# Kernel tuning notes

Hardware: AMD Instinct MI355X
Metric: run time of the kernel (lower is better)

Reference implementation:

```python
import jax, jax.numpy as jnp
import numpy as np

T, B, IN, H = 512, 64, 1024, 1024

def setup_inputs() -> dict:
    key = jax.random.key(0)
    ks = jax.random.split(key, 7)
    X = jax.random.normal(ks[0], (T, B, IN), dtype=jnp.float32)
    h0 = jax.random.normal(ks[1], (B, H), dtype=jnp.float32)
    c0 = jax.random.normal(ks[2], (B, H), dtype=jnp.float32)
    mask = jax.random.randint(ks[3], (T, B), 0, 2, dtype=jnp.int32)
    # orthogonal-ish init approximated with scaled normal (math is identical at runtime)
    W_x_ifoc = jax.random.normal(ks[4], (4 * H, IN), dtype=jnp.float32) / np.sqrt(IN)
    W_h_ifoc = jax.random.normal(ks[5], (4 * H, H), dtype=jnp.float32) / np.sqrt(H)
    b_ifoc = jnp.zeros((4 * H,), dtype=jnp.float32)
    return {"X": X, "h0": h0, "c0": c0, "mask": mask,
            "W_x_ifoc": W_x_ifoc, "W_h_ifoc": W_h_ifoc, "b_ifoc": b_ifoc}

def reference(X, h0, c0, mask, W_x_ifoc, W_h_ifoc, b_ifoc):
    Hd = h0.shape[-1]
    # precompute input projection for all timesteps: [T, B, 4H]
    X4 = jnp.einsum('tbi,gi->tbg', X, W_x_ifoc) + b_ifoc
    m_f = mask.astype(X.dtype)[..., None]  # [T, B, 1]

    def step(carry, inp):
        pre_h, pre_c = carry
        x4, m = inp
        # NOTE: recurrent matmul is applied to the CELL state (non-standard)
        pre = x4 + pre_c @ W_h_ifoc.T  # [B, 4H]
        i, f, o, g = jnp.split(pre, 4, axis=-1)
        i = jax.nn.sigmoid(i)
        f = jax.nn.sigmoid(f)
        o = jax.nn.sigmoid(o)
        c = f * pre_c + i * jnp.tanh(g)
        h = o * jnp.tanh(c)
        h = h * m + pre_h * (1 - m)
        c = c * m + pre_c * (1 - m)
        return (h, c), h

    (h_last, c_last), hiddens = jax.lax.scan(step, (h0, c0), (X4, m_f))
    return hiddens, h_last, c_last
```

## Files before the change

### kernel.cpp

```cpp
#include <hip/hip_runtime.h>
#include <cstdint>
#include <cstddef>

#define T_STEPS 512
#define BATCH   64
#define HD      1024
#define BH      (BATCH * HD)
#define NBLK    256
#define NSG     4
#define BSG     16
#define JBLK    16

using half8   = __attribute__((ext_vector_type(8))) _Float16;
using half4   = __attribute__((ext_vector_type(4))) _Float16;
using floatx4 = __attribute__((ext_vector_type(4))) float;
using float4v = __attribute__((ext_vector_type(4))) float;
using u64     = unsigned long long;

__device__ __forceinline__ float sigmoidf_(float x) { return 1.0f / (1.0f + __expf(-x)); }

__device__ __forceinline__ half8 cvt_h8(float4v a, float4v b) {
    half8 r;
    r[0] = (_Float16)a[0]; r[1] = (_Float16)a[1];
    r[2] = (_Float16)a[2]; r[3] = (_Float16)a[3];
    r[4] = (_Float16)b[0]; r[5] = (_Float16)b[1];
    r[6] = (_Float16)b[2]; r[7] = (_Float16)b[3];
    return r;
}

__device__ __forceinline__ void st_sc1_b64(_Float16* p, u64 v) {
    asm volatile("global_store_dwordx2 %0, %1, off sc0 sc1"
                 :: "v"(p), "v"(v) : "memory");
}

__device__ __forceinline__ u64 pack_lo16(unsigned a, unsigned b, unsigned c, unsigned d) {
    return (u64)(a & 0xffffu) | ((u64)(b & 0xffffu) << 16)
         | ((u64)(c & 0xffffu) << 32) | ((u64)(d & 0xffffu) << 48);
}
__device__ __forceinline__ u64 pack_hi16(unsigned a, unsigned b, unsigned c, unsigned d) {
    return (u64)(a >> 16) | ((u64)(b >> 16) << 16)
         | ((u64)(c >> 16) << 32) | ((u64)(d >> 16) << 48);
}

static const size_t BAR_GRP_OFF  = 0;
static const size_t BAR_ROOT_OFF = 20480;
static const size_t CH_OFF  = 24576;
static const size_t CL_OFF  = CH_OFF + (size_t)2 * BH * 2;
static const size_t WX_OFF  = 1u << 20;
static const size_t WHH_OFF = WX_OFF  + (size_t)8 * 1024 * 1024;
static const size_t WHL_OFF = WHH_OFF + (size_t)8 * 1024 * 1024;
static const size_t XH_OFF  = WHL_OFF + (size_t)8 * 1024 * 1024;
static const size_t X4_OFF  = XH_OFF;
static const size_t TIER_A2_WS = X4_OFF + (size_t)32768 * 4096 * 2;
static const size_t TIER_A_WS  = XH_OFF + (size_t)T_STEPS * BH * 2;
static const size_t TIER_B_WS  = XH_OFF;

__global__ void prep_zero(int* bar) {
    int i = blockIdx.x * 256 + threadIdx.x;
    if (i < 6144) bar[i] = 0;
}

__global__ void prep_w(const float* __restrict__ Wx, const float* __restrict__ Wh,
                       _Float16* __restrict__ wx16,
                       _Float16* __restrict__ whh, _Float16* __restrict__ whl) {
    int i = blockIdx.x * 256 + threadIdx.x;
    if (i < 4 * HD * HD) {
        wx16[i] = (_Float16)Wx[i];
        float w = Wh[i];
        _Float16 h = (_Float16)w;
        whh[i] = h;
        whl[i] = (_Float16)(w - (float)h);
    }
}

__global__ void prep_x(const float* __restrict__ X, _Float16* __restrict__ xh) {
    size_t i = (size_t)blockIdx.x * 256 + threadIdx.x;
    if (i < (size_t)T_STEPS * BH) xh[i] = (_Float16)X[i];
}

__global__ __launch_bounds__(256) void x4_gemm(
    const float* __restrict__ X,
    const _Float16* __restrict__ wx16,
    _Float16* __restrict__ x4)
{
    __shared__ _Float16 sA[128][40];
    __shared__ _Float16 sB[128][40];

    const int tid  = threadIdx.x;
    const int wave = tid >> 6;
    const int lane = tid & 63;
    const int m0 = blockIdx.x * 128, n0 = blockIdx.y * 128;
    const int wm = (wave & 1) * 64,  wn = (wave >> 1) * 64;
    const int fm = lane & 15, q = lane >> 4;

    floatx4 acc[4][4];
    #pragma unroll
    for (int i = 0; i < 4; i++)
        #pragma unroll
        for (int j = 0; j < 4; j++)
            acc[i][j] = (floatx4){0.f, 0.f, 0.f, 0.f};

    for (int k0 = 0; k0 < 1024; k0 += 32) {
        {
            const int kq = (tid & 7) * 4;
            const int rb = tid >> 3;
            #pragma unroll
            for (int it = 0; it < 4; it++) {
                int row = rb + it * 32;
                float4v v = *(const float4v*)(X + (size_t)(m0 + row) * 1024 + k0 + kq);
                half4 h; h[0] = (_Float16)v[0]; h[1] = (_Float16)v[1];
                h[2] = (_Float16)v[2]; h[3] = (_Float16)v[3];
                *(half4*)&sA[row][kq] = h;
            }
        }
        {
            const int half = tid & 1;
            const int row  = tid >> 1;
            const _Float16* src = wx16 + (size_t)(n0 + row) * 1024 + k0 + half * 16;
            *(half8*)&sB[row][half * 16]     = *(const half8*)(src);
            *(half8*)&sB[row][half * 16 + 8] = *(const half8*)(src + 8);
        }
        __syncthreads();

        half8 af[4], bf[4];
        #pragma unroll
        for (int i = 0; i < 4; i++) af[i] = *(const half8*)&sA[wm + 16 * i + fm][q * 8];
        #pragma unroll
        for (int j = 0; j < 4; j++) bf[j] = *(const half8*)&sB[wn + 16 * j + fm][q * 8];
        #pragma unroll
        for (int i = 0; i < 4; i++)
            #pragma unroll
            for (int j = 0; j < 4; j++)
                acc[i][j] = __builtin_amdgcn_mfma_f32_16x16x32_f16(af[i], bf[j], acc[i][j], 0, 0, 0);
        __syncthreads();
    }

    #pragma unroll
    for (int i = 0; i < 4; i++)
        #pragma unroll
        for (int j = 0; j < 4; j++)
            #pragma unroll
            for (int r = 0; r < 4; r++) {
                int row = m0 + wm + 16 * i + q * 4 + r;
                int col = n0 + wn + 16 * j + fm;
                x4[(size_t)row * 4096 + col] = (_Float16)acc[i][j][r];
            }
}

__device__ __forceinline__ void grid_bar(int* grp, int* root, int slot) {
    __syncthreads();
    if (threadIdx.x == 0) {
        int g = blockIdx.x >> 5;
        int v = __hip_atomic_fetch_add(&grp[slot * 8 + g], 1,
                                       __ATOMIC_ACQ_REL, __HIP_MEMORY_SCOPE_AGENT);
        if (v == 31)
            __hip_atomic_fetch_add(&root[slot], 1,
                                   __ATOMIC_ACQ_REL, __HIP_MEMORY_SCOPE_AGENT);
        while (__hip_atomic_load(&root[slot], __ATOMIC_RELAXED,
                                 __HIP_MEMORY_SCOPE_AGENT) < 8)
            __builtin_amdgcn_s_sleep(2);
        (void)__hip_atomic_load(&root[slot], __ATOMIC_ACQUIRE,
                                __HIP_MEMORY_SCOPE_AGENT);
    }
    __syncthreads();
}

__global__ __launch_bounds__(512, 1) void lstm_persist4(
    const _Float16* __restrict__ x4,
    const float* __restrict__ h0, const float* __restrict__ c0,
    const float* __restrict__ bias, const int* __restrict__ mask,
    const _Float16* __restrict__ whh, const _Float16* __restrict__ whl,
    _Float16* __restrict__ chg, _Float16* __restrict__ clg,
    int* __restrict__ bar,
    float* __restrict__ out)
{
    __shared__ float s_pre[8][4][16][18];
    __shared__ float s_h[256], s_c[256];

    const int tid  = threadIdx.x;
    const int wave = tid >> 6;
    const int lane = tid & 63;
    const int sg   = blockIdx.x >> 6;
    const int lb   = blockIdx.x & 63;
    const int b0   = sg * BSG;
    const int j0   = lb * JBLK;

    int*       myflag = bar + (((sg << 6) | lb) << 4);
    const int* pflag  = bar + (((sg << 6) | (wave << 3) | (lane & 7)) << 4);

    const int nn    = lane & 15;
    const int q     = lane >> 4;
    const int kbase = wave * 128 + q * 8;
    const int arow  = lane & 15;

    half8 wh_[4][4], wl_[4][4];
    #pragma unroll
    for (int g = 0; g < 4; g++) {
        const size_t wr = (size_t)(g * HD + j0 + nn) * HD + kbase;
        #pragma unroll
        for (int k = 0; k < 4; k++) {
            wh_[g][k] = *(const half8*)(whh + wr + k * 32);
            wl_[g][k] = *(const half8*)(whl + wr + k * 32);
        }
    }

    float biasr[4] = {0.f, 0.f, 0.f, 0.f};
    float xg[4]    = {0.f, 0.f, 0.f, 0.f};
    int   mv       = 0;
    if (tid < 256) {
        int bl = tid >> 4, n = tid & 15;
        int b = b0 + bl, j = j0 + n;
        float cv = c0[b * HD + j];
        s_c[tid] = cv;
        s_h[tid] = h0[b * HD + j];
        #pragma unroll
        for (int g = 0; g < 4; g++) biasr[g] = bias[g * HD + j];

        _Float16 chi = (_Float16)cv;
        _Float16 clo = (_Float16)(cv - (float)chi);
        unsigned pk = (unsigned)__builtin_bit_cast(unsigned short, chi)
                    | ((unsigned)__builtin_bit_cast(unsigned short, clo) << 16);
        unsigned p1 = __shfl_down(pk, 1);
        unsigned p2 = __shfl_down(pk, 2);
        unsigned p3 = __shfl_down(pk, 3);
        if ((n & 3) == 0) {
            st_sc1_b64(chg + b * HD + j0 + (n & ~3), pack_lo16(pk, p1, p2, p3));
            st_sc1_b64(clg + b * HD + j0 + (n & ~3), pack_hi16(pk, p1, p2, p3));
        }
        #pragma unroll
        for (int g = 0; g < 4; g++)
            xg[g] = (float)x4[(size_t)b * 4096 + g * HD + j];
        mv = mask[b];
        asm volatile("s_waitcnt vmcnt(0)" ::: "memory");
    }
    __syncthreads();
    if (tid == 0)
        __hip_atomic_store(myflag, 1, __ATOMIC_RELAXED, __HIP_MEMORY_SCOPE_AGENT);

    for (int t = 0; t < T_STEPS; t++) {
        const int cur = t & 1;

        const int need = t + 1;
        int fv = __hip_atomic_load(pflag, __ATOMIC_RELAXED, __HIP_MEMORY_SCOPE_AGENT);
        while (!__all(fv >= need)) {
            __builtin_amdgcn_s_sleep(1);
            fv = __hip_atomic_load(pflag, __ATOMIC_RELAXED, __HIP_MEMORY_SCOPE_AGENT);
        }

        const _Float16* chp = chg + (size_t)cur * BH + (size_t)(b0 + arow) * HD + kbase;
        const _Float16* clp = clg + (size_t)cur * BH + (size_t)(b0 + arow) * HD + kbase;

        half8 a0, a1, a2, a3, l0, l1, l2, l3;
        asm volatile(
            "global_load_dwordx4 %0, %8, off sc0 sc1\n\t"
            "global_load_dwordx4 %1, %8, off offset:64 sc0 sc1\n\t"
            "global_load_dwordx4 %2, %8, off offset:128 sc0 sc1\n\t"
            "global_load_dwordx4 %3, %8, off offset:192 sc0 sc1\n\t"
            "global_load_dwordx4 %4, %9, off sc0 sc1\n\t"
            "global_load_dwordx4 %5, %9, off offset:64 sc0 sc1\n\t"
            "global_load_dwordx4 %6, %9, off offset:128 sc0 sc1\n\t"
            "global_load_dwordx4 %7, %9, off offset:192 sc0 sc1\n\t"
            "s_waitcnt vmcnt(0)"
            : "=&v"(a0), "=&v"(a1), "=&v"(a2), "=&v"(a3),
              "=&v"(l0), "=&v"(l1), "=&v"(l2), "=&v"(l3)
            : "v"(chp), "v"(clp)
            : "memory");

        floatx4 acc[4];
        #pragma unroll
        for (int g = 0; g < 4; g++) acc[g] = (floatx4){0.f, 0.f, 0.f, 0.f};
        #pragma unroll
        for (int g = 0; g < 4; g++) {
            floatx4 t0 = acc[g];
            t0 = __builtin_amdgcn_mfma_f32_16x16x32_f16(a0, wh_[g][0], t0, 0, 0, 0);
            t0 = __builtin_amdgcn_mfma_f32_16x16x32_f16(l0, wh_[g][0], t0, 0, 0, 0);
            t0 = __builtin_amdgcn_mfma_f32_16x16x32_f16(a0, wl_[g][0], t0, 0, 0, 0);
            t0 = __builtin_amdgcn_mfma_f32_16x16x32_f16(a1, wh_[g][1], t0, 0, 0, 0);
            t0 = __builtin_amdgcn_mfma_f32_16x16x32_f16(l1, wh_[g][1], t0, 0, 0, 0);
            t0 = __builtin_amdgcn_mfma_f32_16x16x32_f16(a1, wl_[g][1], t0, 0, 0, 0);
            t0 = __builtin_amdgcn_mfma_f32_16x16x32_f16(a2, wh_[g][2], t0, 0, 0, 0);
            t0 = __builtin_amdgcn_mfma_f32_16x16x32_f16(l2, wh_[g][2], t0, 0, 0, 0);
            t0 = __builtin_amdgcn_mfma_f32_16x16x32_f16(a2, wl_[g][2], t0, 0, 0, 0);
            t0 = __builtin_amdgcn_mfma_f32_16x16x32_f16(a3, wh_[g][3], t0, 0, 0, 0);
            t0 = __builtin_amdgcn_mfma_f32_16x16x32_f16(l3, wh_[g][3], t0, 0, 0, 0);
            t0 = __builtin_amdgcn_mfma_f32_16x16x32_f16(a3, wl_[g][3], t0, 0, 0, 0);
            acc[g] = t0;
        }

        #pragma unroll
        for (int g = 0; g < 4; g++) {
            s_pre[wave][g][q * 4 + 0][nn] = acc[g][0];
            s_pre[wave][g][q * 4 + 1][nn] = acc[g][1];
            s_pre[wave][g][q * 4 + 2][nn] = acc[g][2];
            s_pre[wave][g][q * 4 + 3][nn] = acc[g][3];
        }
        __syncthreads();

        float h_out = 0.f, c_out = 0.f;
        if (tid < 256) {
            int bl = tid >> 4, n = tid & 15;
            int b = b0 + bl, j = j0 + n;

            float pg[4];
            #pragma unroll
            for (int g = 0; g < 4; g++) {
                float s = xg[g] + biasr[g];
                #pragma unroll
                for (int kh = 0; kh < 8; kh++)
                    s += s_pre[kh][g][bl][n];
                pg[g] = s;
            }

            float c_old = s_c[tid];
            float i_g = sigmoidf_(pg[0]);
            float f_g = sigmoidf_(pg[1]);
            float o_g = sigmoidf_(pg[2]);
            float g_g = tanhf(pg[3]);
            float c_new = f_g * c_old + i_g * g_g;
            float h_new = o_g * tanhf(c_new);

            h_out = mv ? h_new : s_h[tid];
            c_out = mv ? c_new : c_old;
            s_h[tid] = h_out;
            s_c[tid] = c_out;

            _Float16 chi = (_Float16)c_out;
            _Float16 clo = (_Float16)(c_out - (float)chi);
            unsigned pk = (unsigned)__builtin_bit_cast(unsigned short, chi)
                        | ((unsigned)__builtin_bit_cast(unsigned short, clo) << 16);
            unsigned p1 = __shfl_down(pk, 1);
            unsigned p2 = __shfl_down(pk, 2);
            unsigned p3 = __shfl_down(pk, 3);
            if ((n & 3) == 0) {
                int nxt = cur ^ 1;
                st_sc1_b64(chg + (size_t)nxt * BH + (size_t)b * HD + j0 + (n & ~3),
                           pack_lo16(pk, p1, p2, p3));
                st_sc1_b64(clg + (size_t)nxt * BH + (size_t)b * HD + j0 + (n & ~3),
                           pack_hi16(pk, p1, p2, p3));
            }
            asm volatile("s_waitcnt vmcnt(0)" ::: "memory");
        }
        __syncthreads();
        if (tid == 0)
            __hip_atomic_store(myflag, t + 2, __ATOMIC_RELAXED, __HIP_MEMORY_SCOPE_AGENT);

        if (tid < 256) {
            int bl = tid >> 4, n = tid & 15;
            int b = b0 + bl, j = j0 + n;
            out[(size_t)t * BH + (size_t)b * HD + j] = h_out;
            if (t == T_STEPS - 1) {
                size_t tail = (size_t)T_STEPS * BH;
                out[tail + (size_t)b * HD + j]      = h_out;
                out[tail + BH + (size_t)b * HD + j] = c_out;
            }
            int tn = (t + 1 < T_STEPS) ? t + 1 : t;
            #pragma unroll
            for (int g = 0; g < 4; g++)
                xg[g] = (float)x4[((size_t)tn * BATCH + b) * 4096 + g * HD + j];
            mv = mask[tn * BATCH + b];
        }
    }
}

template<bool XF16>
__global__ __launch_bounds__(1024, 4) void lstm_persist(
    const float* __restrict__ X, const _Float16* __restrict__ xh,
    const float* __restrict__ h0, const float* __restrict__ c0,
    const float* __restrict__ bias, const int* __restrict__ mask,
    const _Float16* __restrict__ wx16, const _Float16* __restrict__ whh,
    const _Float16* __restrict__ whl,
    _Float16* __restrict__ chg, _Float16* __restrict__ clg,
    int* __restrict__ barg, int* __restrict__ barr,
    float* __restrict__ out)
{
    __shared__ _Float16 s_wh[16 * 1032];
    __shared__ float    s_pre[16][16][17];
    __shared__ float    s_h[256], s_c[256];

    const int tid  = threadIdx.x;
    const int wave = tid >> 6;
    const int lane = tid & 63;
    const int j0   = blockIdx.x * 4;

    for (int idx = tid; idx < 2048; idx += 1024) {
        int n  = idx >> 7;
        int kk = (idx & 127) << 3;
        int r  = (n >> 2) * HD + j0 + (n & 3);
        *(half8*)&s_wh[n * 1032 + kk] = *(const half8*)(whh + (size_t)r * HD + kk);
    }

    float biasr[4] = {0.f, 0.f, 0.f, 0.f};
    if (tid < 256) {
        int b = tid >> 2, jj = tid & 3, j = j0 + jj;
        float cv = c0[b * HD + j];
        s_c[tid] = cv;
        s_h[tid] = h0[b * HD + j];
        _Float16 hi = (_Float16)cv;
        chg[b * HD + j] = hi;
        clg[b * HD + j] = (_Float16)(cv - (float)hi);
        #pragma unroll
        for (int g = 0; g < 4; g++) biasr[g] = bias[g * HD + j];
    }
    grid_bar(barg, barr, 0);

    const int mt    = wave & 3;
    const int kh    = wave >> 2;
    const int arow  = mt * 16 + (lane & 15);
    const int nn    = lane & 15;
    const int q     = lane >> 4;
    const int kbase = kh * 256 + q * 8;
    const int wrow  = (nn >> 2) * HD + j0 + (nn & 3);

    const _Float16* wxp = wx16 + (size_t)wrow * HD + kbase;
    const _Float16* wlp = whl  + (size_t)wrow * HD + kbase;
    const _Float16* whp = (const _Float16*)&s_wh[nn * 1032 + kbase];

    for (int t = 0; t < T_STEPS; t++) {
        const int cur = t & 1;
        const _Float16* chp = chg + (size_t)cur * BH + (size_t)arow * HD + kbase;
        const _Float16* clp = clg + (size_t)cur * BH + (size_t)arow * HD + kbase;

        floatx4 acc = {0.f, 0.f, 0.f, 0.f};

        if (XF16) {
            const _Float16* xp = xh + (size_t)t * BH + (size_t)arow * HD + kbase;
            #pragma unroll 4
            for (int k = 0; k < 256; k += 32) {
                half8 av = *(const half8*)(xp + k);
                half8 bv = *(const half8*)(wxp + k);
                acc = __builtin_amdgcn_mfma_f32_16x16x32_f16(av, bv, acc, 0, 0, 0);
            }
        } else {
            const float* xp = X + (size_t)t * BH + (size_t)arow * HD + kbase;
            #pragma unroll 4
            for (int k = 0; k < 256; k += 32) {
                float4v x0 = *(const float4v*)(xp + k);
                float4v x1 = *(const float4v*)(xp + k + 4);
                half8 av = cvt_h8(x0, x1);
                half8 bv = *(const half8*)(wxp + k);
                acc = __builtin_amdgcn_mfma_f32_16x16x32_f16(av, bv, acc, 0, 0, 0);
            }
        }

        #pragma unroll 4
        for (int k = 0; k < 256; k += 32) {
            half8 ah = *(const half8*)(chp + k);
            half8 al = *(const half8*)(clp + k);
            half8 bh = *(const half8*)(whp + k);
            half8 bl = *(const half8*)(wlp + k);
            acc = __builtin_amdgcn_mfma_f32_16x16x32_f16(ah, bh, acc, 0, 0, 0);
            acc = __builtin_amdgcn_mfma_f32_16x16x32_f16(al, bh, acc, 0, 0, 0);
            acc = __builtin_amdgcn_mfma_f32_16x16x32_f16(ah, bl, acc, 0, 0, 0);
        }

        s_pre[wave][q * 4 + 0][nn] = acc[0];
        s_pre[wave][q * 4 + 1][nn] = acc[1];
        s_pre[wave][q * 4 + 2][nn] = acc[2];
        s_pre[wave][q * 4 + 3][nn] = acc[3];
        __syncthreads();

        if (tid < 256) {
            int b = tid >> 2, jj = tid & 3, j = j0 + jj;
            int m = b & 15, mtt = b >> 4;

            float pg[4];
            #pragma unroll
            for (int g = 0; g < 4; g++) {
                float s = 0.f;
                #pragma unroll
                for (int kk = 0; kk < 4; kk++)
                    s += s_pre[kk * 4 + mtt][m][g * 4 + jj];
                pg[g] = s + biasr[g];
            }

            float c_old = s_c[tid];
            float i_g = sigmoidf_(pg[0]);
            float f_g = sigmoidf_(pg[1]);
            float o_g = sigmoidf_(pg[2]);
            float g_g = tanhf(pg[3]);
            float c_new = f_g * c_old + i_g * g_g;
            float h_new = o_g * tanhf(c_new);

            int mv = mask[t * BATCH + b];
            float h_out = mv ? h_new : s_h[tid];
            float c_out = mv ? c_new : c_old;
            s_h[tid] = h_out;
            s_c[tid] = c_out;

            int nxt = cur ^ 1;
            _Float16 hi = (_Float16)c_out;
            chg[(size_t)nxt * BH + b * HD + j] = hi;
            clg[(size_t)nxt * BH + b * HD + j] = (_Float16)(c_out - (float)hi);
            out[(size_t)t * BH + b * HD + j] = h_out;

            if (t == T_STEPS - 1) {
                size_t tail = (size_t)T_STEPS * BH;
                out[tail + b * HD + j]      = h_out;
                out[tail + BH + b * HD + j] = c_out;
            }
        }
        grid_bar(barg, barr, t + 1);
    }
}

__global__ void init_c_fb(const float* __restrict__ c0, float* __restrict__ cf,
                          _Float16* __restrict__ ch, _Float16* __restrict__ cl) {
    int i = blockIdx.x * 256 + threadIdx.x;
    if (i < BH) {
        float v = c0[i];
        cf[i] = v;
        _Float16 h = (_Float16)v;
        ch[i] = h;
        cl[i] = (_Float16)(v - (float)h);
    }
}

__global__ __launch_bounds__(1024) void lstm_step_fb(
    const float* __restrict__ X, const float* __restrict__ h0,
    const float* __restrict__ Wx, const float* __restrict__ Wh,
    const float* __restrict__ bias, const int* __restrict__ mask,
    float* __restrict__ cf, _Float16* __restrict__ chbuf, _Float16* __restrict__ clbuf,
    float* __restrict__ out, int t)
{
    __shared__ float lds_pre[4][64][16];
    const int tid = threadIdx.x, wave = tid >> 6, lane = tid & 63;
    const int g = wave & 3, mt = wave >> 2, j0 = blockIdx.x * 16;
    const int cur = t & 1;
    const float* cf_prev = cf + (size_t)cur * BH;
    const _Float16* ch_prev = chbuf + (size_t)cur * BH;
    const _Float16* cl_prev = clbuf + (size_t)cur * BH;
    float* cf_next = cf + (size_t)(cur ^ 1) * BH;
    _Float16* ch_next = chbuf + (size_t)(cur ^ 1) * BH;
    _Float16* cl_next = clbuf + (size_t)(cur ^ 1) * BH;
    const int arow = mt * 16 + (lane & 15);
    const int brow = g * HD + j0 + (lane & 15);
    const int koff = (lane >> 4) * 8;
    floatx4 acc = {0.f, 0.f, 0.f, 0.f};
    {
        const float* xp = X + (size_t)t * BH + (size_t)arow * HD + koff;
        const float* wp = Wx + (size_t)brow * HD + koff;
        #pragma unroll 4
        for (int k = 0; k < HD; k += 32) {
            float4v x0 = *(const float4v*)(xp + k);
            float4v x1 = *(const float4v*)(xp + k + 4);
            float4v w0 = *(const float4v*)(wp + k);
            float4v w1 = *(const float4v*)(wp + k + 4);
            acc = __builtin_amdgcn_mfma_f32_16x16x32_f16(cvt_h8(x0, x1), cvt_h8(w0, w1), acc, 0, 0, 0);
        }
    }
    {
        const _Float16* chp = ch_prev + (size_t)arow * HD + koff;
        const _Float16* clp = cl_prev + (size_t)arow * HD + koff;
        const float* whp = Wh + (size_t)brow * HD + koff;
        #pragma unroll 4
        for (int k = 0; k < HD; k += 32) {
            half8 ah = *(const half8*)(chp + k);
            half8 al = *(const half8*)(clp + k);
            float4v w0 = *(const float4v*)(whp + k);
            float4v w1 = *(const float4v*)(whp + k + 4);
            half8 bh = cvt_h8(w0, w1);
            float4v r0, r1;
            r0[0] = w0[0] - (float)bh[0]; r0[1] = w0[1] - (float)bh[1];
            r0[2] = w0[2] - (float)bh[2]; r0[3] = w0[3] - (float)bh[3];
            r1[0] = w1[0] - (float)bh[4]; r1[1] = w1[1] - (float)bh[5];
            r1[2] = w1[2] - (float)bh[6]; r1[3] = w1[3] - (float)bh[7];
            half8 bl = cvt_h8(r0, r1);
            acc = __builtin_amdgcn_mfma_f32_16x16x32_f16(ah, bh, acc, 0, 0, 0);
            acc = __builtin_amdgcn_mfma_f32_16x16x32_f16(al, bh, acc, 0, 0, 0);
            acc = __builtin_amdgcn_mfma_f32_16x16x32_f16(ah, bl, acc, 0, 0, 0);
        }
    }
    {
        const int qq = lane >> 4, col = lane & 15;
        lds_pre[g][mt * 16 + qq * 4 + 0][col] = acc[0];
        lds_pre[g][mt * 16 + qq * 4 + 1][col] = acc[1];
        lds_pre[g][mt * 16 + qq * 4 + 2][col] = acc[2];
        lds_pre[g][mt * 16 + qq * 4 + 3][col] = acc[3];
    }
    __syncthreads();
    {
        const int bl2 = tid >> 4, n = tid & 15, j = j0 + n;
        float pg[4];
        #pragma unroll
        for (int gg = 0; gg < 4; gg++) pg[gg] = lds_pre[gg][bl2][n] + bias[gg * HD + j];
        float c_old = cf_prev[bl2 * HD + j];
        float i_g = sigmoidf_(pg[0]), f_g = sigmoidf_(pg[1]);
        float o_g = sigmoidf_(pg[2]), g_g = tanhf(pg[3]);
        float c_new = f_g * c_old + i_g * g_g;
        float h_new = o_g * tanhf(c_new);
        int mv = mask[t * BATCH + bl2];
        float h_prev = (t == 0) ? h0[bl2 * HD + j] : out[(size_t)(t - 1) * BH + bl2 * HD + j];
        float h_out = mv ? h_new : h_prev;
        float c_out = mv ? c_new : c_old;
        cf_next[bl2 * HD + j] = c_out;
        _Float16 hh = (_Float16)c_out;
        ch_next[bl2 * HD + j] = hh;
        cl_next[bl2 * HD + j] = (_Float16)(c_out - (float)hh);
        out[(size_t)t * BH + bl2 * HD + j] = h_out;
        if (t == T_STEPS - 1) {
            size_t tail = (size_t)T_STEPS * BH;
            out[tail + bl2 * HD + j] = h_out;
            out[tail + BH + bl2 * HD + j] = c_out;
        }
    }
}

extern "C" void kernel_launch(void* const* d_in, const int* in_sizes, int n_in,
                              void* d_out, int out_size, void* d_ws, size_t ws_size,
                              hipStream_t stream) {
    const float* X    = (const float*)d_in[0];
    const float* h0   = (const float*)d_in[1];
    const float* c0   = (const float*)d_in[2];
    const int*   mask = (const int*)  d_in[3];
    const float* Wx   = (const float*)d_in[4];
    const float* Wh   = (const float*)d_in[5];
    const float* bias = (const float*)d_in[6];
    float* out = (float*)d_out;
    char* ws = (char*)d_ws;

    if (ws_size >= TIER_B_WS) {
        int*      barg = (int*)(ws + BAR_GRP_OFF);
        int*      barr = (int*)(ws + BAR_ROOT_OFF);
        _Float16* chg  = (_Float16*)(ws + CH_OFF);
        _Float16* clg  = (_Float16*)(ws + CL_OFF);
        _Float16* wx16 = (_Float16*)(ws + WX_OFF);
        _Float16* whh  = (_Float16*)(ws + WHH_OFF);
        _Float16* whl  = (_Float16*)(ws + WHL_OFF);

        prep_zero<<<dim3(24), dim3(256), 0, stream>>>(barg);
        prep_w<<<dim3(16384), dim3(256), 0, stream>>>(Wx, Wh, wx16, whh, whl);

        if (ws_size >= TIER_A2_WS) {
            _Float16* x4 = (_Float16*)(ws + X4_OFF);
            x4_gemm<<<dim3(256, 32), dim3(256), 0, stream>>>(X, wx16, x4);
            void* args[] = {
                (void*)&x4, (void*)&h0, (void*)&c0, (void*)&bias, (void*)&mask,
                (void*)&whh, (void*)&whl, (void*)&chg, (void*)&clg,
                (void*)&barg, (void*)&out
            };
            hipLaunchCooperativeKernel((const void*)&lstm_persist4,
                                       dim3(NBLK), dim3(512), args, 0, stream);
        } else {
            _Float16* xh = (_Float16*)(ws + XH_OFF);
            const bool tierA = ws_size >= TIER_A_WS;
            if (tierA)
                prep_x<<<dim3(131072), dim3(256), 0, stream>>>(X, xh);
            void* args[] = {
                (void*)&X, (void*)&xh, (void*)&h0, (void*)&c0, (void*)&bias,
                (void*)&mask, (void*)&wx16, (void*)&whh, (void*)&whl,
                (void*)&chg, (void*)&clg, (void*)&barg, (void*)&barr, (void*)&out
            };
            if (tierA)
                hipLaunchCooperativeKernel((const void*)&lstm_persist<true>,
                                           dim3(NBLK), dim3(1024), args, 0, stream);
            else
                hipLaunchCooperativeKernel((const void*)&lstm_persist<false>,
                                           dim3(NBLK), dim3(1024), args, 0, stream);
        }
    } else {
        float*    cf = (float*)ws;
        _Float16* ch = (_Float16*)(ws + 524288);
        _Float16* cl = (_Float16*)(ws + 786432);
        init_c_fb<<<dim3((BH + 255) / 256), dim3(256), 0, stream>>>(c0, cf, ch, cl);
        for (int t = 0; t < T_STEPS; t++)
            lstm_step_fb<<<dim3(64), dim3(1024), 0, stream>>>(
                X, h0, Wx, Wh, bias, mask, cf, ch, cl, out, t);
    }
}
```

Before: 3.169 ms.

## Replace per-step flag barrier with parity-tagged cell-state data polling

Removes the per-block flag stores, the flag spin-wait and the trailing __syncthreads/vmcnt wait from each timestep. Instead, the low mantissa bit of each fp16 hi/lo cell value carries the step parity, and consumers poll the data itself until every word shows the expected parity. A triple-buffered interleaved hi/lo state array and double-buffered LDS partials make this safe, and a poison kernel initialises the buffers. The cost is one mantissa bit of precision in each half of the split cell state, plus repeated polling loads of the full operand.

New measurement: 4.087 ms. 1.29x slower.

```diff
diff --git a/kernel.cpp b/kernel.cpp
--- a/kernel.cpp
+++ b/kernel.cpp
@@ -10,11 +10,13 @@
 #define NSG     4
 #define BSG     16
 #define JBLK    16
+#define CBYTES  ((size_t)BH * 4)
 
 using half8   = __attribute__((ext_vector_type(8))) _Float16;
 using half4   = __attribute__((ext_vector_type(4))) _Float16;
 using floatx4 = __attribute__((ext_vector_type(4))) float;
 using float4v = __attribute__((ext_vector_type(4))) float;
+using int4v   = __attribute__((ext_vector_type(4))) int;
 using u64     = unsigned long long;
 
 __device__ __forceinline__ float sigmoidf_(float x) { return 1.0f / (1.0f + __expf(-x)); }
@@ -28,11 +30,6 @@
     return r;
 }
 
-__device__ __forceinline__ void st_sc1_b64(_Float16* p, u64 v) {
-    asm volatile("global_store_dwordx2 %0, %1, off sc0 sc1"
-                 :: "v"(p), "v"(v) : "memory");
-}
-
 __device__ __forceinline__ u64 pack_lo16(unsigned a, unsigned b, unsigned c, unsigned d) {
     return (u64)(a & 0xffffu) | ((u64)(b & 0xffffu) << 16)
          | ((u64)(c & 0xffffu) << 32) | ((u64)(d & 0xffffu) << 48);
@@ -40,6 +37,15 @@
 __device__ __forceinline__ u64 pack_hi16(unsigned a, unsigned b, unsigned c, unsigned d) {
     return (u64)(a >> 16) | ((u64)(b >> 16) << 16)
          | ((u64)(c >> 16) << 32) | ((u64)(d >> 16) << 48);
+}
+
+__device__ __forceinline__ unsigned tag_pack(float c, unsigned p) {
+    unsigned hb = (unsigned)__builtin_bit_cast(unsigned short, (_Float16)c);
+    hb = (hb & 0xFFFEu) | p;
+    _Float16 hf = __builtin_bit_cast(_Float16, (unsigned short)hb);
+    unsigned lb = (unsigned)__builtin_bit_cast(unsigned short, (_Float16)(c - (float)hf));
+    lb = (lb & 0xFFFEu) | p;
+    return hb | (lb << 16);
 }
 
 static const size_t BAR_GRP_OFF  = 0;
@@ -58,6 +64,14 @@
 __global__ void prep_zero(int* bar) {
     int i = blockIdx.x * 256 + threadIdx.x;
     if (i < 6144) bar[i] = 0;
+}
+
+__global__ void prep_poison(unsigned* c3) {
+    int i = blockIdx.x * 256 + threadIdx.x;
+    if (i < 196608) {
+        int buf = i >> 16;
+        c3[i] = (buf == 1) ? 0u : 0x00010001u;
+    }
 }
 
 __global__ void prep_w(const float* __restrict__ Wx, const float* __restrict__ Wh,
@@ -165,16 +179,15 @@
     __syncthreads();
 }
 
-__global__ __launch_bounds__(512, 1) void lstm_persist4(
+__global__ __launch_bounds__(512, 1) void lstm_persist5(
     const _Float16* __restrict__ x4,
     const float* __restrict__ h0, const float* __restrict__ c0,
     const float* __restrict__ bias, const int* __restrict__ mask,
     const _Float16* __restrict__ whh, const _Float16* __restrict__ whl,
-    _Float16* __restrict__ chg, _Float16* __restrict__ clg,
-    int* __restrict__ bar,
+    char* __restrict__ c3,
     float* __restrict__ out)
 {
-    __shared__ float s_pre[8][4][16][18];
+    __shared__ float s_pre[2][8][4][16][18];
     __shared__ float s_h[256], s_c[256];
 
     const int tid  = threadIdx.x;
@@ -184,9 +197,6 @@
     const int lb   = blockIdx.x & 63;
     const int b0   = sg * BSG;
     const int j0   = lb * JBLK;
-
-    int*       myflag = bar + (((sg << 6) | lb) << 4);
-    const int* pflag  = bar + (((sg << 6) | (wave << 3) | (lane & 7)) << 4);
 
     const int nn    = lane & 15;
     const int q     = lane >> 4;
@@ -216,55 +226,71 @@
         #pragma unroll
         for (int g = 0; g < 4; g++) biasr[g] = bias[g * HD + j];
 
-        _Float16 chi = (_Float16)cv;
-        _Float16 clo = (_Float16)(cv - (float)chi);
-        unsigned pk = (unsigned)__builtin_bit_cast(unsigned short, chi)
-                    | ((unsigned)__builtin_bit_cast(unsigned short, clo) << 16);
+        unsigned pk = tag_pack(cv, 0u);
         unsigned p1 = __shfl_down(pk, 1);
         unsigned p2 = __shfl_down(pk, 2);
         unsigned p3 = __shfl_down(pk, 3);
         if ((n & 3) == 0) {
-            st_sc1_b64(chg + b * HD + j0 + (n & ~3), pack_lo16(pk, p1, p2, p3));
-            st_sc1_b64(clg + b * HD + j0 + (n & ~3), pack_hi16(pk, p1, p2, p3));
+            union { u64 qv[2]; int4v v; } sv;
+            sv.qv[0] = pack_lo16(pk, p1, p2, p3);
+            sv.qv[1] = pack_hi16(pk, p1, p2, p3);
+            char* wp = c3 + ((size_t)b * HD + j0 + n) * 4;
+            asm volatile("global_store_dwordx4 %0, %1, off sc0 sc1"
+                         :: "v"(wp), "v"(sv.v) : "memory");
         }
         #pragma unroll
         for (int g = 0; g < 4; g++)
             xg[g] = (float)x4[(size_t)b * 4096 + g * HD + j];
         mv = mask[b];
-        asm volatile("s_waitcnt vmcnt(0)" ::: "memory");
-    }
-    __syncthreads();
-    if (tid == 0)
-        __hip_atomic_store(myflag, 1, __ATOMIC_RELAXED, __HIP_MEMORY_SCOPE_AGENT);
-
+    }
+
+    int bi = 0;
     for (int t = 0; t < T_STEPS; t++) {
-        const int cur = t & 1;
-
-        const int need = t + 1;
-        int fv = __hip_atomic_load(pflag, __ATOMIC_RELAXED, __HIP_MEMORY_SCOPE_AGENT);
-        while (!__all(fv >= need)) {
-            __builtin_amdgcn_s_sleep(1);
-            fv = __hip_atomic_load(pflag, __ATOMIC_RELAXED, __HIP_MEMORY_SCOPE_AGENT);
-        }
-
-        const _Float16* chp = chg + (size_t)cur * BH + (size_t)(b0 + arow) * HD + kbase;
-        const _Float16* clp = clg + (size_t)cur * BH + (size_t)(b0 + arow) * HD + kbase;
-
-        half8 a0, a1, a2, a3, l0, l1, l2, l3;
-        asm volatile(
-            "global_load_dwordx4 %0, %8, off sc0 sc1\n\t"
-            "global_load_dwordx4 %1, %8, off offset:64 sc0 sc1\n\t"
-            "global_load_dwordx4 %2, %8, off offset:128 sc0 sc1\n\t"
-            "global_load_dwordx4 %3, %8, off offset:192 sc0 sc1\n\t"
-            "global_load_dwordx4 %4, %9, off sc0 sc1\n\t"
-            "global_load_dwordx4 %5, %9, off offset:64 sc0 sc1\n\t"
-            "global_load_dwordx4 %6, %9, off offset:128 sc0 sc1\n\t"
-            "global_load_dwordx4 %7, %9, off offset:192 sc0 sc1\n\t"
-            "s_waitcnt vmcnt(0)"
-            : "=&v"(a0), "=&v"(a1), "=&v"(a2), "=&v"(a3),
-              "=&v"(l0), "=&v"(l1), "=&v"(l2), "=&v"(l3)
-            : "v"(chp), "v"(clp)
-            : "memory");
+        const int pp = t & 1;
+        const unsigned pat = pp ? 0x00010001u : 0u;
+
+        int4v u0, u1, u2, u3, u4, u5, u6, u7;
+        const char* cp = c3 + (size_t)bi * CBYTES
+                       + ((size_t)(b0 + arow) * HD + kbase) * 4;
+        for (;;) {
+            asm volatile(
+                "global_load_dwordx4 %0, %8, off sc0 sc1\n\t"
+                "global_load_dwordx4 %1, %8, off offset:16 sc0 sc1\n\t"
+                "global_load_dwordx4 %2, %8, off offset:128 sc0 sc1\n\t"
+                "global_load_dwordx4 %3, %8, off offset:144 sc0 sc1\n\t"
+                "global_load_dwordx4 %4, %8, off offset:256 sc0 sc1\n\t"
+                "global_load_dwordx4 %5, %8, off offset:272 sc0 sc1\n\t"
+                "global_load_dwordx4 %6, %8, off offset:384 sc0 sc1\n\t"
+                "global_load_dwordx4 %7, %8, off offset:400 sc0 sc1\n\t"
+                "s_waitcnt vmcnt(0)"
+                : "=&v"(u0), "=&v"(u1), "=&v"(u2), "=&v"(u3),
+                  "=&v"(u4), "=&v"(u5), "=&v"(u6), "=&v"(u7)
+                : "v"(cp) : "memory");
+            unsigned accv =
+                ((unsigned)u0[0] ^ pat) | ((unsigned)u0[1] ^ pat) | ((unsigned)u0[2] ^ pat) | ((unsigned)u0[3] ^ pat) |
+                ((unsigned)u1[0] ^ pat) | ((unsigned)u1[1] ^ pat) | ((unsigned)u1[2] ^ pat) | ((unsigned)u1[3] ^ pat) |
+                ((unsigned)u2[0] ^ pat) | ((unsigned)u2[1] ^ pat) | ((unsigned)u2[2] ^ pat) | ((unsigned)u2[3] ^ pat) |
+                ((unsigned)u3[0] ^ pat) | ((unsigned)u3[1] ^ pat) | ((unsigned)u3[2] ^ pat) | ((unsigned)u3[3] ^ pat) |
+                ((unsigned)u4[0] ^ pat) | ((unsigned)u4[1] ^ pat) | ((unsigned)u4[2] ^ pat) | ((unsigned)u4[3] ^ pat) |
+                ((unsigned)u5[0] ^ pat) | ((unsigned)u5[1] ^ pat) | ((unsigned)u5[2] ^ pat) | ((unsigned)u5[3] ^ pat) |
+                ((unsigned)u6[0] ^ pat) | ((unsigned)u6[1] ^ pat) | ((unsigned)u6[2] ^ pat) | ((unsigned)u6[3] ^ pat) |
+                ((unsigned)u7[0] ^ pat) | ((unsigned)u7[1] ^ pat) | ((unsigned)u7[2] ^ pat) | ((unsigned)u7[3] ^ pat);
+            if (__all((accv & 0x00010001u) == 0u)) break;
+            __builtin_amdgcn_s_sleep(8);
+        }
+
+        union C4 { int4v i; half8 h; };
+        C4 ca0, ca1, ca2, ca3, cl0, cl1, cl2, cl3;
+        ca0.i = (int4v){u0[0], u0[1], u1[0], u1[1]};
+        cl0.i = (int4v){u0[2], u0[3], u1[2], u1[3]};
+        ca1.i = (int4v){u2[0], u2[1], u3[0], u3[1]};
+        cl1.i = (int4v){u2[2], u2[3], u3[2], u3[3]};
+        ca2.i = (int4v){u4[0], u4[1], u5[0], u5[1]};
+        cl2.i = (int4v){u4[2], u4[3], u5[2], u5[3]};
+        ca3.i = (int4v){u6[0], u6[1], u7[0], u7[1]};
+        cl3.i = (int4v){u6[2], u6[3], u7[2], u7[3]};
+        half8 a0 = ca0.h, a1 = ca1.h, a2 = ca2.h, a3 = ca3.h;
+        half8 l0 = cl0.h, l1 = cl1.h, l2 = cl2.h, l3 = cl3.h;
 
         floatx4 acc[4];
         #pragma unroll
@@ -289,14 +315,14 @@
 
         #pragma unroll
         for (int g = 0; g < 4; g++) {
-            s_pre[wave][g][q * 4 + 0][nn] = acc[g][0];
-            s_pre[wave][g][q * 4 + 1][nn] = acc[g][1];
-            s_pre[wave][g][q * 4 + 2][nn] = acc[g][2];
-            s_pre[wave][g][q * 4 + 3][nn] = acc[g][3];
+            s_pre[pp][wave][g][q * 4 + 0][nn] = acc[g][0];
+            s_pre[pp][wave][g][q * 4 + 1][nn] = acc[g][1];
+            s_pre[pp][wave][g][q * 4 + 2][nn] = acc[g][2];
+            s_pre[pp][wave][g][q * 4 + 3][nn] = acc[g][3];
         }
         __syncthreads();
 
-        float h_out = 0.f, c_out = 0.f;
+        const int wi = (bi == 2) ? 0 : bi + 1;
         if (tid < 256) {
             int bl = tid >> 4, n = tid & 15;
             int b = b0 + bl, j = j0 + n;
@@ -307,7 +333,7 @@
                 float s = xg[g] + biasr[g];
                 #pragma unroll
                 for (int kh = 0; kh < 8; kh++)
-                    s += s_pre[kh][g][bl][n];
+                    s += s_pre[pp][kh][g][bl][n];
                 pg[g] = s;
             }
 
@@ -319,46 +345,38 @@
             float c_new = f_g * c_old + i_g * g_g;
             float h_new = o_g * tanhf(c_new);
 
-            h_out = mv ? h_new : s_h[tid];
-            c_out = mv ? c_new : c_old;
+            float h_out = mv ? h_new : s_h[tid];
+            float c_out = mv ? c_new : c_old;
             s_h[tid] = h_out;
             s_c[tid] = c_out;
 
-            _Float16 chi = (_Float16)c_out;
-            _Float16 clo = (_Float16)(c_out - (float)chi);
-            unsigned pk = (unsigned)__builtin_bit_cast(unsigned short, chi)
-                        | ((unsigned)__builtin_bit_cast(unsigned short, clo) << 16);
+            unsigned pk = tag_pack(c_out, (unsigned)((t + 1) & 1));
             unsigned p1 = __shfl_down(pk, 1);
             unsigned p2 = __shfl_down(pk, 2);
             unsigned p3 = __shfl_down(pk, 3);
             if ((n & 3) == 0) {
-                int nxt = cur ^ 1;
-                st_sc1_b64(chg + (size_t)nxt * BH + (size_t)b * HD + j0 + (n & ~3),
-                           pack_lo16(pk, p1, p2, p3));
-                st_sc1_b64(clg + (size_t)nxt * BH + (size_t)b * HD + j0 + (n & ~3),
-                           pack_hi16(pk, p1, p2, p3));
-            }
-            asm volatile("s_waitcnt vmcnt(0)" ::: "memory");
-        }
-        __syncthreads();
-        if (tid == 0)
-            __hip_atomic_store(myflag, t + 2, __ATOMIC_RELAXED, __HIP_MEMORY_SCOPE_AGENT);
-
-        if (tid < 256) {
-            int bl = tid >> 4, n = tid & 15;
-            int b = b0 + bl, j = j0 + n;
+                union { u64 qv[2]; int4v v; } sv;
+                sv.qv[0] = pack_lo16(pk, p1, p2, p3);
+                sv.qv[1] = pack_hi16(pk, p1, p2, p3);
+                char* wp = c3 + (size_t)wi * CBYTES + ((size_t)b * HD + j0 + n) * 4;
+                asm volatile("global_store_dwordx4 %0, %1, off sc0 sc1"
+                             :: "v"(wp), "v"(sv.v) : "memory");
+            }
+
             out[(size_t)t * BH + (size_t)b * HD + j] = h_out;
             if (t == T_STEPS - 1) {
                 size_t tail = (size_t)T_STEPS * BH;
                 out[tail + (size_t)b * HD + j]      = h_out;
                 out[tail + BH + (size_t)b * HD + j] = c_out;
             }
+
             int tn = (t + 1 < T_STEPS) ? t + 1 : t;
             #pragma unroll
             for (int g = 0; g < 4; g++)
                 xg[g] = (float)x4[((size_t)tn * BATCH + b) * 4096 + g * HD + j];
             mv = mask[tn * BATCH + b];
         }
+        bi = wi;
     }
 }
 
@@ -563,7 +581,8 @@
             r0[0] = w0[0] - (float)bh[0]; r0[1] = w0[1] - (float)bh[1];
             r0[2] = w0[2] - (float)bh[2]; r0[3] = w0[3] - (float)bh[3];
             r1[0] = w1[0] - (float)bh[4]; r1[1] = w1[1] - (float)bh[5];
-            r1[2] = w1[2] - (float)bh[6]; r1[3] = w1[3] - (float)bh[7];
+            r1[2] = w1[2] - (float)bh[6]; r1[3] = w1[7 - 7] - (float)bh[7];
+            r1[3] = w1[3] - (float)bh[7];
             half8 bl = cvt_h8(r0, r1);
             acc = __builtin_amdgcn_mfma_f32_16x16x32_f16(ah, bh, acc, 0, 0, 0);
             acc = __builtin_amdgcn_mfma_f32_16x16x32_f16(al, bh, acc, 0, 0, 0);
@@ -627,20 +646,21 @@
         _Float16* whh  = (_Float16*)(ws + WHH_OFF);
         _Float16* whl  = (_Float16*)(ws + WHL_OFF);
 
-        prep_zero<<<dim3(24), dim3(256), 0, stream>>>(barg);
         prep_w<<<dim3(16384), dim3(256), 0, stream>>>(Wx, Wh, wx16, whh, whl);
 
         if (ws_size >= TIER_A2_WS) {
+            char* c3 = ws + CH_OFF;
             _Float16* x4 = (_Float16*)(ws + X4_OFF);
+            prep_poison<<<dim3(768), dim3(256), 0, stream>>>((unsigned*)c3);
             x4_gemm<<<dim3(256, 32), dim3(256), 0, stream>>>(X, wx16, x4);
             void* args[] = {
                 (void*)&x4, (void*)&h0, (void*)&c0, (void*)&bias, (void*)&mask,
-                (void*)&whh, (void*)&whl, (void*)&chg, (void*)&clg,
-                (void*)&barg, (void*)&out
+                (void*)&whh, (void*)&whl, (void*)&c3, (void*)&out
             };
-            hipLaunchCooperativeKernel((const void*)&lstm_persist4,
+            hipLaunchCooperativeKernel((const void*)&lstm_persist5,
                                        dim3(NBLK), dim3(512), args, 0, stream);
         } else {
+            prep_zero<<<dim3(24), dim3(256), 0, stream>>>(barg);
             _Float16* xh = (_Float16*)(ws + XH_OFF);
             const bool tierA = ws_size >= TIER_A_WS;
             if (tierA)
```
